# Optimization experiments

Hardware: AMD Instinct MI355X
Metric: run time of the kernel (lower is better)

## Reference

```python
import jax, jax.numpy as jnp
import numpy as np

N_NODES = 50000
N_EDGES = 1_600_000


def add_self_loops(edge_index, n):
    loops = jnp.arange(n, dtype=edge_index.dtype)
    return jnp.concatenate([edge_index, jnp.stack([loops, loops])], axis=1)


def gat_layer(x, edge_index, W, a_src, a_dst, b):
    """PyG GATConv (concat=True, negative_slope=0.2, add_self_loops handled by caller)."""
    src, dst = edge_index[0], edge_index[1]
    n = x.shape[0]
    H, C = a_src.shape
    xp = (x @ W).reshape(n, H, C)                       # [N,H,C] transformed features
    al_src = jnp.einsum('nhc,hc->nh', xp, a_src)        # [N,H]
    al_dst = jnp.einsum('nhc,hc->nh', xp, a_dst)        # [N,H]
    logits = jax.nn.leaky_relu(al_src[src] + al_dst[dst], negative_slope=0.2)  # [E,H]
    m = jax.lax.stop_gradient(jax.ops.segment_max(logits, dst, num_segments=n))
    e = jnp.exp(logits - m[dst])                        # stable segment softmax
    denom = jax.ops.segment_sum(e, dst, num_segments=n)
    alpha = e / denom[dst]                              # [E,H]
    out = jax.ops.segment_sum(xp[src] * alpha[:, :, None], dst, num_segments=n)  # [N,H,C]
    return out.reshape(n, H * C) + b


def setup_inputs() -> dict:
    key = jax.random.key(0)
    ks = jax.random.split(key, 11)
    s = 0.1  # weight scale
    return {
        'x': jax.random.normal(ks[0], (N_NODES, 128), jnp.float32),
        'edge_index': jax.random.randint(ks[1], (2, N_EDGES), 0, N_NODES, jnp.int32),
        'W1': s * jax.random.normal(ks[2], (128, 128), jnp.float32),
        'a_src1': s * jax.random.normal(ks[3], (2, 64), jnp.float32),
        'a_dst1': s * jax.random.normal(ks[4], (2, 64), jnp.float32),
        'b1': s * jax.random.normal(ks[5], (128,), jnp.float32),
        'W2': s * jax.random.normal(ks[6], (128, 64), jnp.float32),
        'a_src2': s * jax.random.normal(ks[7], (2, 32), jnp.float32),
        'a_dst2': s * jax.random.normal(ks[8], (2, 32), jnp.float32),
        'b2': s * jax.random.normal(ks[9], (64,), jnp.float32),
    }


def reference(x, edge_index, W1, a_src1, a_dst1, b1, W2, a_src2, a_dst2, b2):
    ei = add_self_loops(edge_index, x.shape[0])
    encoded = x  # FeatureEncoding with no auxiliary features: identity passthrough
    h = jax.nn.elu(gat_layer(encoded, ei, W1, a_src1, a_dst1, b1))
    out = jax.nn.elu(gat_layer(h, ei, W2, a_src2, a_dst2, b2))
    return (out, encoded)
```

## Files before the change

### kernel.cpp

```cpp
#include <hip/hip_runtime.h>
#include <math.h>

#define N_NODES 50000
#define N_EDGES 1600000
#define EA (N_EDGES + N_NODES)
#define MAXD 128
#define NBUCK 196
#define EPB 4096
#define BCAP 16000

typedef unsigned int uint32;
typedef float f32x4 __attribute__((ext_vector_type(4)));
typedef _Float16 h16x2 __attribute__((ext_vector_type(2)));
typedef _Float16 f16x8 __attribute__((ext_vector_type(8)));

__device__ inline h16x2 u2h(uint32 u) { return __builtin_bit_cast(h16x2, u); }
__device__ inline uint32 h2u(h16x2 h) { return __builtin_bit_cast(uint32, h); }
__device__ inline uint32 pkh(float a, float b) {
  return __builtin_bit_cast(uint32, __builtin_amdgcn_cvt_pkrtz(a, b));
}
__device__ inline ushort f2h(float f) {
  _Float16 h = (_Float16)f;
  return __builtin_bit_cast(ushort, h);
}
__device__ inline int clampi(int v, int lo, int hi) {
  return v < lo ? lo : (v > hi ? hi : v);
}

template<int N, bool AF16, bool COPYX, bool HBLK>
__global__ __launch_bounds__(256) void gemm_mfma_kernel(
    const void* __restrict__ Ap, const float* __restrict__ B,
    const float* __restrict__ asrc, const float* __restrict__ adst,
    ushort* __restrict__ Cb, float* __restrict__ al, float* __restrict__ encout, int M) {
  constexpr int KK = 4;
  constexpr int NC = N / 16;
  constexpr int NH = N / 2;
  __shared__ uint32 Bl[KK * NC * 64 * 4];
  const int t = threadIdx.x;

  for (int id = t; id < KK * NC * 64; id += 256) {
    int lane = id & 63;
    int cf = (id >> 6) % NC;
    int kk = (id >> 6) / NC;
    int col = cf * 16 + (lane & 15);
    int k0 = kk * 32 + (lane >> 4) * 8;
    uint32 w0 = pkh(B[(k0 + 0) * N + col], B[(k0 + 1) * N + col]);
    uint32 w1 = pkh(B[(k0 + 2) * N + col], B[(k0 + 3) * N + col]);
    uint32 w2 = pkh(B[(k0 + 4) * N + col], B[(k0 + 5) * N + col]);
    uint32 w3 = pkh(B[(k0 + 6) * N + col], B[(k0 + 7) * N + col]);
    *reinterpret_cast<uint4*>(&Bl[id * 4]) = make_uint4(w0, w1, w2, w3);
  }
  __syncthreads();

  const int w = t >> 6, lane = t & 63;
  const int l15 = lane & 15, g4 = lane >> 4;
  const int row0 = blockIdx.x * 64 + w * 16;
  int arow = row0 + l15; if (arow > M - 1) arow = M - 1;
  const int k0 = g4 * 8;

  f32x4 acc[NC];
#pragma unroll
  for (int c = 0; c < NC; ++c) acc[c] = f32x4{0.f, 0.f, 0.f, 0.f};

#pragma unroll
  for (int kk = 0; kk < KK; ++kk) {
    f16x8 af;
    if (AF16) {
      int kabs = kk * 32 + k0;
      int kh = kabs >= 64;
      af = *reinterpret_cast<const f16x8*>(
          (const ushort*)Ap + (size_t)kh * N_NODES * 64 + (size_t)arow * 64 + (kabs - kh * 64));
    } else {
      const float* A = (const float*)Ap;
      float4 a0 = *reinterpret_cast<const float4*>(A + (size_t)arow * 128 + kk * 32 + k0);
      float4 a1 = *reinterpret_cast<const float4*>(A + (size_t)arow * 128 + kk * 32 + k0 + 4);
      if (COPYX) {
        *reinterpret_cast<float4*>(encout + (size_t)arow * 128 + kk * 32 + k0)     = a0;
        *reinterpret_cast<float4*>(encout + (size_t)arow * 128 + kk * 32 + k0 + 4) = a1;
      }
      union { uint32 u[4]; f16x8 v; } p;
      p.u[0] = pkh(a0.x, a0.y);
      p.u[1] = pkh(a0.z, a0.w);
      p.u[2] = pkh(a1.x, a1.y);
      p.u[3] = pkh(a1.z, a1.w);
      af = p.v;
    }
#pragma unroll
    for (int c = 0; c < NC; ++c) {
      f16x8 bf = *reinterpret_cast<const f16x8*>(&Bl[((kk * NC + c) * 64 + lane) * 4]);
      acc[c] = __builtin_amdgcn_mfma_f32_16x16x32_f16(af, bf, acc[c], 0, 0, 0);
    }
  }

  float as_c[NC], ad_c[NC];
#pragma unroll
  for (int c = 0; c < NC; ++c) { as_c[c] = asrc[c * 16 + l15]; ad_c[c] = adst[c * 16 + l15]; }
#pragma unroll
  for (int reg = 0; reg < 4; ++reg) {
    int row = row0 + g4 * 4 + reg;
    bool ok = row < M;
    float ps0 = 0.f, ps1 = 0.f, pd0 = 0.f, pd1 = 0.f;
#pragma unroll
    for (int c = 0; c < NC; ++c) {
      float v = acc[c][reg];
      if (ok) {
        int col = c * 16 + l15;
        if (HBLK) {
          int ch = col >= NH;
          Cb[(size_t)ch * N_NODES * NH + (size_t)row * NH + (col - ch * NH)] = f2h(v);
        } else {
          Cb[(size_t)row * N + col] = f2h(v);
        }
      }
      if (c < NC / 2) { ps0 += v * as_c[c]; pd0 += v * ad_c[c]; }
      else            { ps1 += v * as_c[c]; pd1 += v * ad_c[c]; }
    }
#pragma unroll
    for (int off = 8; off >= 1; off >>= 1) {
      ps0 += __shfl_xor(ps0, off); ps1 += __shfl_xor(ps1, off);
      pd0 += __shfl_xor(pd0, off); pd1 += __shfl_xor(pd1, off);
    }
    if (ok && l15 == 0) {
      if (HBLK) {
        ((float2*)al)[row]           = make_float2(ps0, pd0);
        ((float2*)al)[N_NODES + row] = make_float2(ps1, pd1);
      } else {
        *reinterpret_cast<float4*>(&al[row * 4]) = make_float4(ps0, ps1, pd0, pd1);
      }
    }
  }
}

__global__ void partA_kernel(const int* __restrict__ src, const int* __restrict__ dst,
                             int* __restrict__ bcur, uint32* __restrict__ ebuf) {
  __shared__ int h[NBUCK];
  __shared__ int lo[NBUCK];
  __shared__ int rank_[NBUCK];
  __shared__ uint32 staged[EPB];
  const int t = threadIdx.x;
  const int e0 = blockIdx.x * EPB;
  const int ne = min(EPB, N_EDGES - e0);

  for (int i = t; i < NBUCK; i += 256) h[i] = 0;
  __syncthreads();
  for (int i = t; i < ne; i += 256) {
    int d = dst[e0 + i];
    atomicAdd(&h[d >> 8], 1);
  }
  __syncthreads();
  if (t == 0) {
    int a = 0;
    for (int b = 0; b < NBUCK; ++b) { lo[b] = a; a += h[b]; }
  }
  __syncthreads();
  for (int i = t; i < NBUCK; i += 256) rank_[i] = lo[i];
  __syncthreads();
  for (int i = t; i < ne; i += 256) {
    int d = dst[e0 + i];
    int s = src[e0 + i];
    int b = d >> 8;
    int r = atomicAdd(&rank_[b], 1);
    staged[r] = ((uint32)b << 24) | ((uint32)s << 8) | (uint32)(d & 255);
  }
  __syncthreads();
  if (t < NBUCK) {
    int old = atomicAdd(&bcur[t], h[t]);
    rank_[t] = t * BCAP + old - lo[t];
  }
  __syncthreads();
  for (int i = t; i < ne; i += 256) {
    uint32 wd = staged[i];
    ebuf[rank_[wd >> 24] + i] = wd;
  }
}

__global__ __launch_bounds__(256) void partB2_kernel(
    const int* __restrict__ bcur, const uint32* __restrict__ ebuf,
    int* __restrict__ row_start, int* __restrict__ sorted_src) {
  __shared__ uint32 sl[BCAP];
  __shared__ int h[256];
  __shared__ int cur[256];
  __shared__ int wsh[4];
  __shared__ int red[4];
  const int b = blockIdx.x;
  const int t = threadIdx.x, lane = t & 63, wv = t >> 6;
  int myv = 0;
  if (t < b) myv = bcur[t] + min(256, N_NODES - t * 256);
  for (int off = 32; off >= 1; off >>= 1) myv += __shfl_xor(myv, off);
  if (lane == 0) red[wv] = myv;
  h[t] = 0;
  __syncthreads();
  const int bbase = red[0] + red[1] + red[2] + red[3];
  const int base = b * BCAP;
  const int len = min(bcur[b], BCAP);
  for (int i = t; i < len; i += 256) {
    uint32 w = ebuf[base + i];
    sl[i] = w;
    atomicAdd(&h[w & 255], 1);
  }
  __syncthreads();
  const int n = b * 256 + t;
  const bool valid = n < N_NODES;
  int v = valid ? h[t] + 1 : 0;
  int x = v;
  for (int off = 1; off < 64; off <<= 1) {
    int y = __shfl_up(x, off);
    if (lane >= off) x += y;
  }
  if (lane == 63) wsh[wv] = x;
  __syncthreads();
  int wo = 0;
  for (int w = 0; w < wv; ++w) wo += wsh[w];
  int rs = bbase + wo + x - v;
  if (valid) {
    row_start[n] = rs;
    sorted_src[rs] = n;
    cur[t] = rs + 1;
  }
  if (b == 0 && t == 0) row_start[N_NODES] = EA;
  __syncthreads();
  for (int i = t; i < len; i += 256) {
    uint32 w = sl[i];
    int pos = atomicAdd(&cur[w & 255], 1);
    sorted_src[pos] = (int)((w >> 8) & 0xffffu);
  }
}

template<int HCH>
__global__ __launch_bounds__(256) void agg_split_kernel(
    const ushort* __restrict__ xh, const float* __restrict__ al,
    const int* __restrict__ row_start, const int* __restrict__ sorted_src,
    const float* __restrict__ bias, ushort* __restrict__ outp) {
  constexpr int RSH = HCH / 2;
  constexpr int LPR = HCH / 8;
  constexpr int EPI = 64 / LPR;
  constexpr int PF  = 32 / EPI;
  __shared__ uint2 pL[4][MAXD];
  const int gw = (blockIdx.x * blockDim.x + threadIdx.x) >> 6;
  const int lane = threadIdx.x & 63;
  const int wv = (threadIdx.x >> 6) & 3;
  if (gw >= 2 * N_NODES) return;
  const int head = gw >= N_NODES ? 1 : 0;
  const int node = gw - head * N_NODES;
  const float2* alh = (const float2*)al + (size_t)head * N_NODES;
  const uint32* xb32 = (const uint32*)xh + (size_t)head * N_NODES * RSH;
  int start = row_start[node], end = row_start[node + 1];
  start = clampi(start, 0, EA);
  end   = clampi(end, start, EA);
  const int deg = end - start;
  const float adh = alh[node].y;
  const float ESH = 2.7725887f;
  float dsum = 0.f;

  if (deg > MAXD) {
    float m = -1e30f;
    for (int i = start + lane; i < end; i += 64) {
      int s = clampi(sorted_src[i], 0, N_NODES - 1);
      float l = alh[s].x + adh; l = l > 0.f ? l : 0.2f * l;
      m = fmaxf(m, l);
    }
    for (int off = 32; off >= 1; off >>= 1) m = fmaxf(m, __shfl_xor(m, off));
    for (int i = start + lane; i < end; i += 64) {
      int s = clampi(sorted_src[i], 0, N_NODES - 1);
      float l = alh[s].x + adh; l = l > 0.f ? l : 0.2f * l;
      dsum += __expf(l - m);
    }
    for (int off = 32; off >= 1; off >>= 1) dsum += __shfl_xor(dsum, off);
    const float inv = 1.f / dsum;
    if (lane < RSH) {
      float a0 = 0.f, a1 = 0.f;
      for (int i = start; i < end; ++i) {
        int s = clampi(sorted_src[i], 0, N_NODES - 1);
        float l = alh[s].x + adh; l = l > 0.f ? l : 0.2f * l;
        float w = __expf(l - m) * inv;
        h16x2 hx = u2h(xb32[(size_t)s * RSH + lane]);
        a0 = fmaf(w, (float)hx[0], a0);
        a1 = fmaf(w, (float)hx[1], a1);
      }
      int cols0 = head * HCH + lane * 2;
      float o0 = a0 + bias[cols0];
      float o1 = a1 + bias[cols0 + 1];
      o0 = o0 > 0.f ? o0 : __expf(o0) - 1.f;
      o1 = o1 > 0.f ? o1 : __expf(o1) - 1.f;
      ((uint32*)outp)[(size_t)head * N_NODES * RSH + (size_t)node * RSH + lane] = pkh(o0, o1);
    }
    return;
  }

  for (int i = start + lane; i < end; i += 64) {
    int s = clampi(sorted_src[i], 0, N_NODES - 1);
    float l = alh[s].x + adh; l = l > 0.f ? l : 0.2f * l;
    float e = __expf(l - ESH);
    pL[wv][i - start] = make_uint2((uint32)s, pkh(e, e));
    dsum += e;
  }

  const int q  = lane / LPR;
  const int cc = lane % LPR;
  const uint2* myP = &pL[wv][0];
  const uint32* myx = xb32 + cc * 4;

  uint4 pv[PF];
  h16x2 pw[PF];
#pragma unroll
  for (int st = 0; st < PF; ++st) {
    int jj = st * EPI + q;
    int jc = jj < deg ? jj : 0;
    uint2 p = myP[jc];
    pw[st] = u2h(jj < deg ? p.y : 0u);
    pv[st] = *reinterpret_cast<const uint4*>(myx + (size_t)p.x * RSH);
  }

  for (int off = 32; off >= 1; off >>= 1) dsum += __shfl_xor(dsum, off);
  const float inv = 1.f / dsum;

  h16x2 acc2[4];
#pragma unroll
  for (int k = 0; k < 4; ++k) acc2[k] = u2h(0u);

#pragma unroll
  for (int st = 0; st < PF; ++st) {
    acc2[0] += pw[st] * u2h(pv[st].x); acc2[1] += pw[st] * u2h(pv[st].y);
    acc2[2] += pw[st] * u2h(pv[st].z); acc2[3] += pw[st] * u2h(pv[st].w);
  }

  int j = PF * EPI;
  for (; j + 2 * EPI <= deg; j += 2 * EPI) {
    uint2 p0 = myP[j + q];
    uint2 p1 = myP[j + EPI + q];
    const uint4 v0 = *reinterpret_cast<const uint4*>(myx + (size_t)p0.x * RSH);
    const uint4 v1 = *reinterpret_cast<const uint4*>(myx + (size_t)p1.x * RSH);
    h16x2 w0 = u2h(p0.y), w1 = u2h(p1.y);
    acc2[0] += w0 * u2h(v0.x); acc2[1] += w0 * u2h(v0.y);
    acc2[2] += w0 * u2h(v0.z); acc2[3] += w0 * u2h(v0.w);
    acc2[0] += w1 * u2h(v1.x); acc2[1] += w1 * u2h(v1.y);
    acc2[2] += w1 * u2h(v1.z); acc2[3] += w1 * u2h(v1.w);
  }
  for (; j < deg; j += EPI) {
    int jj = j + q;
    int jc = jj < deg ? jj : 0;
    uint2 p = myP[jc];
    h16x2 w2 = u2h(jj < deg ? p.y : 0u);
    const uint4 v = *reinterpret_cast<const uint4*>(myx + (size_t)p.x * RSH);
    acc2[0] += w2 * u2h(v.x); acc2[1] += w2 * u2h(v.y);
    acc2[2] += w2 * u2h(v.z); acc2[3] += w2 * u2h(v.w);
  }

#pragma unroll
  for (int k = 0; k < 4; ++k) {
#pragma unroll
    for (int off = LPR; off < 64; off <<= 1)
      acc2[k] = u2h((uint32)__shfl_xor((int)h2u(acc2[k]), off)) + acc2[k];
  }

  if (q == 0) {
    float o[8];
#pragma unroll
    for (int k = 0; k < 4; ++k) {
      o[2 * k]     = (float)acc2[k][0] * inv + bias[head * HCH + cc * 8 + 2 * k];
      o[2 * k + 1] = (float)acc2[k][1] * inv + bias[head * HCH + cc * 8 + 2 * k + 1];
    }
#pragma unroll
    for (int k = 0; k < 8; ++k) o[k] = o[k] > 0.f ? o[k] : __expf(o[k]) - 1.f;
    uint4 u;
    u.x = pkh(o[0], o[1]); u.y = pkh(o[2], o[3]);
    u.z = pkh(o[4], o[5]); u.w = pkh(o[6], o[7]);
    *reinterpret_cast<uint4*>((uint32*)outp + (size_t)head * N_NODES * RSH +
                              (size_t)node * RSH + cc * 4) = u;
  }
}

__global__ __launch_bounds__(256) void agg_full_kernel(
    const ushort* __restrict__ xh, const float* __restrict__ al,
    const int* __restrict__ row_start, const int* __restrict__ sorted_src,
    const float* __restrict__ bias, float* __restrict__ outp) {
  constexpr int HC = 64;
  constexpr int LPR = HC / 8;
  constexpr int EPI = 64 / LPR;
  constexpr int RS  = HC / 2;
  constexpr int PF  = 4;
  __shared__ uint2 pL[4][2][MAXD];
  const int wid = (blockIdx.x * blockDim.x + threadIdx.x) >> 6;
  const int lane = threadIdx.x & 63;
  const int wv = (threadIdx.x >> 6) & 3;
  if (wid >= N_NODES) return;
  const float4* al4 = (const float4*)al;
  const uint32* xb32 = (const uint32*)xh;
  int start = row_start[wid], end = row_start[wid + 1];
  start = clampi(start, 0, EA);
  end   = clampi(end, start, EA);
  const int deg = end - start;
  float4 mya = al4[wid];
  const float ad0 = mya.z, ad1 = mya.w;
  const float ESH = 2.7725887f;
  float d0 = 0.f, d1 = 0.f;

  if (deg > MAXD) {
    float m0 = -1e30f, m1 = -1e30f;
    for (int i = start + lane; i < end; i += 64) {
      int s = clampi(sorted_src[i], 0, N_NODES - 1);
      float4 a = al4[s];
      float l0 = a.x + ad0; l0 = l0 > 0.f ? l0 : 0.2f * l0;
      float l1 = a.y + ad1; l1 = l1 > 0.f ? l1 : 0.2f * l1;
      m0 = fmaxf(m0, l0); m1 = fmaxf(m1, l1);
    }
    for (int off = 32; off >= 1; off >>= 1) {
      m0 = fmaxf(m0, __shfl_xor(m0, off));
      m1 = fmaxf(m1, __shfl_xor(m1, off));
    }
    for (int i = start + lane; i < end; i += 64) {
      int s = clampi(sorted_src[i], 0, N_NODES - 1);
      float4 a = al4[s];
      float l0 = a.x + ad0; l0 = l0 > 0.f ? l0 : 0.2f * l0;
      float l1 = a.y + ad1; l1 = l1 > 0.f ? l1 : 0.2f * l1;
      d0 += __expf(l0 - m0); d1 += __expf(l1 - m1);
    }
    for (int off = 32; off >= 1; off >>= 1) {
      d0 += __shfl_xor(d0, off);
      d1 += __shfl_xor(d1, off);
    }
    const float inv0 = 1.f / d0, inv1 = 1.f / d1;
    const int cols0 = lane * 2;
    const int head = cols0 >= 32;
    const float invh = head ? inv1 : inv0;
    const float mh = head ? m1 : m0;
    const float adh = head ? ad1 : ad0;
    float a0 = 0.f, a1 = 0.f;
    if (lane < RS) {
      for (int i = start; i < end; ++i) {
        int s = clampi(sorted_src[i], 0, N_NODES - 1);
        float lv = (head ? al4[s].y : al4[s].x) + adh;
        lv = lv > 0.f ? lv : 0.2f * lv;
        float w = __expf(lv - mh) * invh;
        h16x2 hx = u2h(xb32[(size_t)s * RS + lane]);
        a0 = fmaf(w, (float)hx[0], a0);
        a1 = fmaf(w, (float)hx[1], a1);
      }
      float o0 = a0 + bias[cols0];
      float o1 = a1 + bias[cols0 + 1];
      o0 = o0 > 0.f ? o0 : __expf(o0) - 1.f;
      o1 = o1 > 0.f ? o1 : __expf(o1) - 1.f;
      *reinterpret_cast<float2*>(outp + (size_t)wid * HC + cols0) = make_float2(o0, o1);
    }
    return;
  }

  for (int i = start + lane; i < end; i += 64) {
    int s = clampi(sorted_src[i], 0, N_NODES - 1);
    float4 a = al4[s];
    float l0 = a.x + ad0; l0 = l0 > 0.f ? l0 : 0.2f * l0;
    float l1 = a.y + ad1; l1 = l1 > 0.f ? l1 : 0.2f * l1;
    float e0 = __expf(l0 - ESH);
    float e1 = __expf(l1 - ESH);
    int j = i - start;
    pL[wv][0][j] = make_uint2((uint32)s, pkh(e0, e0));
    pL[wv][1][j] = make_uint2((uint32)s, pkh(e1, e1));
    d0 += e0; d1 += e1;
  }

  const int q  = lane / LPR;
  const int cc = lane % LPR;
  const int hd = cc / (LPR / 2);
  const uint2* myP = &pL[wv][hd][0];
  const uint32* myx = xb32 + cc * 4;

  uint4 pv[PF];
  h16x2 pw[PF];
#pragma unroll
  for (int st = 0; st < PF; ++st) {
    int jj = st * EPI + q;
    int jc = jj < deg ? jj : 0;
    uint2 p = myP[jc];
    pw[st] = u2h(jj < deg ? p.y : 0u);
    pv[st] = *reinterpret_cast<const uint4*>(myx + (size_t)p.x * RS);
  }

  for (int off = 32; off >= 1; off >>= 1) {
    d0 += __shfl_xor(d0, off);
    d1 += __shfl_xor(d1, off);
  }
  const float inv0 = 1.f / d0, inv1 = 1.f / d1;

  h16x2 acc2[4];
#pragma unroll
  for (int k = 0; k < 4; ++k) acc2[k] = u2h(0u);

#pragma unroll
  for (int st = 0; st < PF; ++st) {
    acc2[0] += pw[st] * u2h(pv[st].x); acc2[1] += pw[st] * u2h(pv[st].y);
    acc2[2] += pw[st] * u2h(pv[st].z); acc2[3] += pw[st] * u2h(pv[st].w);
  }

  int j = PF * EPI;
  for (; j + 2 * EPI <= deg; j += 2 * EPI) {
    uint2 p0 = myP[j + q];
    uint2 p1 = myP[j + EPI + q];
    const uint4 v0 = *reinterpret_cast<const uint4*>(myx + (size_t)p0.x * RS);
    const uint4 v1 = *reinterpret_cast<const uint4*>(myx + (size_t)p1.x * RS);
    h16x2 w0 = u2h(p0.y), w1 = u2h(p1.y);
    acc2[0] += w0 * u2h(v0.x); acc2[1] += w0 * u2h(v0.y);
    acc2[2] += w0 * u2h(v0.z); acc2[3] += w0 * u2h(v0.w);
    acc2[0] += w1 * u2h(v1.x); acc2[1] += w1 * u2h(v1.y);
    acc2[2] += w1 * u2h(v1.z); acc2[3] += w1 * u2h(v1.w);
  }
  for (; j < deg; j += EPI) {
    int jj = j + q;
    int jc = jj < deg ? jj : 0;
    uint2 p = myP[jc];
    h16x2 w2 = u2h(jj < deg ? p.y : 0u);
    const uint4 v = *reinterpret_cast<const uint4*>(myx + (size_t)p.x * RS);
    acc2[0] += w2 * u2h(v.x); acc2[1] += w2 * u2h(v.y);
    acc2[2] += w2 * u2h(v.z); acc2[3] += w2 * u2h(v.w);
  }

#pragma unroll
  for (int k = 0; k < 4; ++k) {
#pragma unroll
    for (int off = LPR; off < 64; off <<= 1)
      acc2[k] = u2h((uint32)__shfl_xor((int)h2u(acc2[k]), off)) + acc2[k];
  }

  if (q == 0) {
    const float invh = hd ? inv1 : inv0;
    float o[8];
#pragma unroll
    for (int k = 0; k < 4; ++k) {
      o[2 * k]     = (float)acc2[k][0] * invh + bias[cc * 8 + 2 * k];
      o[2 * k + 1] = (float)acc2[k][1] * invh + bias[cc * 8 + 2 * k + 1];
    }
#pragma unroll
    for (int k = 0; k < 8; ++k) o[k] = o[k] > 0.f ? o[k] : __expf(o[k]) - 1.f;
    float* op = outp + (size_t)wid * HC + cc * 8;
    *reinterpret_cast<float4*>(op)     = make_float4(o[0], o[1], o[2], o[3]);
    *reinterpret_cast<float4*>(op + 4) = make_float4(o[4], o[5], o[6], o[7]);
  }
}

extern "C" void kernel_launch(void* const* d_in, const int* in_sizes, int n_in,
                              void* d_out, int out_size, void* d_ws, size_t ws_size,
                              hipStream_t stream) {
  const float* x      = (const float*)d_in[0];
  const int*   ei     = (const int*)d_in[1];
  const float* W1     = (const float*)d_in[2];
  const float* a_src1 = (const float*)d_in[3];
  const float* a_dst1 = (const float*)d_in[4];
  const float* b1     = (const float*)d_in[5];
  const float* W2     = (const float*)d_in[6];
  const float* a_src2 = (const float*)d_in[7];
  const float* a_dst2 = (const float*)d_in[8];
  const float* b2     = (const float*)d_in[9];
  float* out = (float*)d_out;

  char* ws = (char*)d_ws;
  size_t off = 0;
  auto alloc = [&](size_t bytes) {
    void* p = ws + off;
    off = (off + bytes + 255) & ~(size_t)255;
    return p;
  };
  ushort* xh1       = (ushort*)alloc((size_t)N_NODES * 128 * 2);
  ushort* h1h       = (ushort*)alloc((size_t)N_NODES * 128 * 2);
  ushort* xh2       = (ushort*)alloc((size_t)N_NODES * 64 * 2);
  float*  al1       = (float*)alloc((size_t)N_NODES * 4 * 4);
  float*  al2       = (float*)alloc((size_t)N_NODES * 4 * 4);
  int*    row_start = (int*)alloc((size_t)(N_NODES + 1) * 4);
  int*    bcur      = (int*)alloc(NBUCK * 4);
  int*    sorted_src= (int*)alloc((size_t)EA * 4);
  uint32* ebuf      = (uint32*)h1h;

  const int* src = ei;
  const int* dst = ei + N_EDGES;

  const int agg1Blocks = (2 * N_NODES * 64) / 256;
  const int agg2Blocks = (N_NODES * 64) / 256;
  const int partBlocks = (N_EDGES + EPB - 1) / EPB;
  const int gemmBlocks = (N_NODES + 63) / 64;

  hipMemsetAsync(bcur, 0, NBUCK * 4, stream);
  partA_kernel<<<partBlocks, 256, 0, stream>>>(src, dst, bcur, ebuf);
  partB2_kernel<<<NBUCK, 256, 0, stream>>>(bcur, ebuf, row_start, sorted_src);

  gemm_mfma_kernel<128, false, true, true><<<gemmBlocks, 256, 0, stream>>>(
      x, W1, a_src1, a_dst1, xh1, al1, out + (size_t)N_NODES * 64, N_NODES);
  agg_split_kernel<64><<<agg1Blocks, 256, 0, stream>>>(xh1, al1, row_start, sorted_src, b1, h1h);

  gemm_mfma_kernel<64, true, false, false><<<gemmBlocks, 256, 0, stream>>>(
      h1h, W2, a_src2, a_dst2, xh2, al2, nullptr, N_NODES);
  agg_full_kernel<<<agg2Blocks, 256, 0, stream>>>(xh2, al2, row_start, sorted_src, b2, out);
}
```

Measured before the change: 155.2 us.

## Keep per-edge indices and weights in registers via shuffles instead of LDS

For nodes with degree up to 64, each lane now holds one edge's source index and packed softmax weight in registers, and the gather loop broadcasts them with wave shuffles instead of staging them in shared memory. This drops the LDS arrays, cuts LDS traffic and the LDS footprint that limited occupancy, and fully unrolls the gather into at most two batches of four loads per lane. The slow fallback threshold drops from 128 to 64, so nodes with degree between 65 and 128 now take the slower per-lane serial path. Leaky-relu is also rewritten as a single fmaxf.

```diff
diff --git a/kernel.cpp b/kernel.cpp
--- a/kernel.cpp
+++ b/kernel.cpp
@@ -4,7 +4,6 @@
 #define N_NODES 50000
 #define N_EDGES 1600000
 #define EA (N_EDGES + N_NODES)
-#define MAXD 128
 #define NBUCK 196
 #define EPB 4096
 #define BCAP 16000
@@ -234,11 +233,8 @@
   constexpr int RSH = HCH / 2;
   constexpr int LPR = HCH / 8;
   constexpr int EPI = 64 / LPR;
-  constexpr int PF  = 32 / EPI;
-  __shared__ uint2 pL[4][MAXD];
   const int gw = (blockIdx.x * blockDim.x + threadIdx.x) >> 6;
   const int lane = threadIdx.x & 63;
-  const int wv = (threadIdx.x >> 6) & 3;
   if (gw >= 2 * N_NODES) return;
   const int head = gw >= N_NODES ? 1 : 0;
   const int node = gw - head * N_NODES;
@@ -250,19 +246,18 @@
   const int deg = end - start;
   const float adh = alh[node].y;
   const float ESH = 2.7725887f;
-  float dsum = 0.f;
-
-  if (deg > MAXD) {
-    float m = -1e30f;
+
+  if (deg > 64) {
+    float m = -1e30f, dsum = 0.f;
     for (int i = start + lane; i < end; i += 64) {
       int s = clampi(sorted_src[i], 0, N_NODES - 1);
-      float l = alh[s].x + adh; l = l > 0.f ? l : 0.2f * l;
+      float l = alh[s].x + adh; l = fmaxf(l, 0.2f * l);
       m = fmaxf(m, l);
     }
     for (int off = 32; off >= 1; off >>= 1) m = fmaxf(m, __shfl_xor(m, off));
     for (int i = start + lane; i < end; i += 64) {
       int s = clampi(sorted_src[i], 0, N_NODES - 1);
-      float l = alh[s].x + adh; l = l > 0.f ? l : 0.2f * l;
+      float l = alh[s].x + adh; l = fmaxf(l, 0.2f * l);
       dsum += __expf(l - m);
     }
     for (int off = 32; off >= 1; off >>= 1) dsum += __shfl_xor(dsum, off);
@@ -271,7 +266,7 @@
       float a0 = 0.f, a1 = 0.f;
       for (int i = start; i < end; ++i) {
         int s = clampi(sorted_src[i], 0, N_NODES - 1);
-        float l = alh[s].x + adh; l = l > 0.f ? l : 0.2f * l;
+        float l = alh[s].x + adh; l = fmaxf(l, 0.2f * l);
         float w = __expf(l - m) * inv;
         h16x2 hx = u2h(xb32[(size_t)s * RSH + lane]);
         a0 = fmaf(w, (float)hx[0], a0);
@@ -287,70 +282,77 @@
     return;
   }
 
-  for (int i = start + lane; i < end; i += 64) {
-    int s = clampi(sorted_src[i], 0, N_NODES - 1);
-    float l = alh[s].x + adh; l = l > 0.f ? l : 0.2f * l;
-    float e = __expf(l - ESH);
-    pL[wv][i - start] = make_uint2((uint32)s, pkh(e, e));
-    dsum += e;
-  }
+  uint32 s_reg = 0, wpk = 0;
+  float e = 0.f;
+  {
+    int i = start + lane;
+    if (i < end) {
+      int s = clampi(sorted_src[i], 0, N_NODES - 1);
+      s_reg = (uint32)s;
+      float l = alh[s].x + adh;
+      l = fmaxf(l, 0.2f * l);
+      e = __expf(l - ESH);
+      wpk = pkh(e, e);
+    }
+  }
+  float dsum = e;
+  for (int off = 32; off >= 1; off >>= 1) dsum += __shfl_xor(dsum, off);
+  const float inv = 1.f / dsum;
 
   const int q  = lane / LPR;
   const int cc = lane % LPR;
-  const uint2* myP = &pL[wv][0];
   const uint32* myx = xb32 + cc * 4;
 
-  uint4 pv[PF];
-  h16x2 pw[PF];
-#pragma unroll
-  for (int st = 0; st < PF; ++st) {
-    int jj = st * EPI + q;
-    int jc = jj < deg ? jj : 0;
-    uint2 p = myP[jc];
-    pw[st] = u2h(jj < deg ? p.y : 0u);
-    pv[st] = *reinterpret_cast<const uint4*>(myx + (size_t)p.x * RSH);
-  }
-
-  for (int off = 32; off >= 1; off >>= 1) dsum += __shfl_xor(dsum, off);
-  const float inv = 1.f / dsum;
-
   h16x2 acc2[4];
 #pragma unroll
   for (int k = 0; k < 4; ++k) acc2[k] = u2h(0u);
 
-#pragma unroll
-  for (int st = 0; st < PF; ++st) {
-    acc2[0] += pw[st] * u2h(pv[st].x); acc2[1] += pw[st] * u2h(pv[st].y);
-    acc2[2] += pw[st] * u2h(pv[st].z); acc2[3] += pw[st] * u2h(pv[st].w);
-  }
-
-  int j = PF * EPI;
-  for (; j + 2 * EPI <= deg; j += 2 * EPI) {
-    uint2 p0 = myP[j + q];
-    uint2 p1 = myP[j + EPI + q];
-    const uint4 v0 = *reinterpret_cast<const uint4*>(myx + (size_t)p0.x * RSH);
-    const uint4 v1 = *reinterpret_cast<const uint4*>(myx + (size_t)p1.x * RSH);
-    h16x2 w0 = u2h(p0.y), w1 = u2h(p1.y);
-    acc2[0] += w0 * u2h(v0.x); acc2[1] += w0 * u2h(v0.y);
-    acc2[2] += w0 * u2h(v0.z); acc2[3] += w0 * u2h(v0.w);
-    acc2[0] += w1 * u2h(v1.x); acc2[1] += w1 * u2h(v1.y);
-    acc2[2] += w1 * u2h(v1.z); acc2[3] += w1 * u2h(v1.w);
-  }
-  for (; j < deg; j += EPI) {
-    int jj = j + q;
-    int jc = jj < deg ? jj : 0;
-    uint2 p = myP[jc];
-    h16x2 w2 = u2h(jj < deg ? p.y : 0u);
-    const uint4 v = *reinterpret_cast<const uint4*>(myx + (size_t)p.x * RSH);
-    acc2[0] += w2 * u2h(v.x); acc2[1] += w2 * u2h(v.y);
-    acc2[2] += w2 * u2h(v.z); acc2[3] += w2 * u2h(v.w);
+  {
+    int b0 = q, b1 = q + EPI, b2 = q + 2 * EPI, b3 = q + 3 * EPI;
+    uint32 s0 = (uint32)__shfl((int)s_reg, b0), w0 = (uint32)__shfl((int)wpk, b0);
+    uint32 s1 = (uint32)__shfl((int)s_reg, b1), w1 = (uint32)__shfl((int)wpk, b1);
+    uint32 s2 = (uint32)__shfl((int)s_reg, b2), w2 = (uint32)__shfl((int)wpk, b2);
+    uint32 s3 = (uint32)__shfl((int)s_reg, b3), w3 = (uint32)__shfl((int)wpk, b3);
+    const uint4 v0 = *reinterpret_cast<const uint4*>(myx + (size_t)s0 * RSH);
+    const uint4 v1 = *reinterpret_cast<const uint4*>(myx + (size_t)s1 * RSH);
+    const uint4 v2 = *reinterpret_cast<const uint4*>(myx + (size_t)s2 * RSH);
+    const uint4 v3 = *reinterpret_cast<const uint4*>(myx + (size_t)s3 * RSH);
+    h16x2 h0 = u2h(w0), h1 = u2h(w1), h2 = u2h(w2), h3 = u2h(w3);
+    acc2[0] += h0 * u2h(v0.x); acc2[1] += h0 * u2h(v0.y);
+    acc2[2] += h0 * u2h(v0.z); acc2[3] += h0 * u2h(v0.w);
+    acc2[0] += h1 * u2h(v1.x); acc2[1] += h1 * u2h(v1.y);
+    acc2[2] += h1 * u2h(v1.z); acc2[3] += h1 * u2h(v1.w);
+    acc2[0] += h2 * u2h(v2.x); acc2[1] += h2 * u2h(v2.y);
+    acc2[2] += h2 * u2h(v2.z); acc2[3] += h2 * u2h(v2.w);
+    acc2[0] += h3 * u2h(v3.x); acc2[1] += h3 * u2h(v3.y);
+    acc2[2] += h3 * u2h(v3.z); acc2[3] += h3 * u2h(v3.w);
+  }
+  if (deg > 32) {
+    int b0 = 32 + q, b1 = 40 + q, b2 = 48 + q, b3 = 56 + q;
+    uint32 s0 = (uint32)__shfl((int)s_reg, b0), w0 = (uint32)__shfl((int)wpk, b0);
+    uint32 s1 = (uint32)__shfl((int)s_reg, b1), w1 = (uint32)__shfl((int)wpk, b1);
+    uint32 s2 = (uint32)__shfl((int)s_reg, b2), w2 = (uint32)__shfl((int)wpk, b2);
+    uint32 s3 = (uint32)__shfl((int)s_reg, b3), w3 = (uint32)__shfl((int)wpk, b3);
+    const uint4 v0 = *reinterpret_cast<const uint4*>(myx + (size_t)s0 * RSH);
+    const uint4 v1 = *reinterpret_cast<const uint4*>(myx + (size_t)s1 * RSH);
+    const uint4 v2 = *reinterpret_cast<const uint4*>(myx + (size_t)s2 * RSH);
+    const uint4 v3 = *reinterpret_cast<const uint4*>(myx + (size_t)s3 * RSH);
+    h16x2 h0 = u2h(w0), h1 = u2h(w1), h2 = u2h(w2), h3 = u2h(w3);
+    acc2[0] += h0 * u2h(v0.x); acc2[1] += h0 * u2h(v0.y);
+    acc2[2] += h0 * u2h(v0.z); acc2[3] += h0 * u2h(v0.w);
+    acc2[0] += h1 * u2h(v1.x); acc2[1] += h1 * u2h(v1.y);
+    acc2[2] += h1 * u2h(v1.z); acc2[3] += h1 * u2h(v1.w);
+    acc2[0] += h2 * u2h(v2.x); acc2[1] += h2 * u2h(v2.y);
+    acc2[2] += h2 * u2h(v2.z); acc2[3] += h2 * u2h(v2.w);
+    acc2[0] += h3 * u2h(v3.x); acc2[1] += h3 * u2h(v3.y);
+    acc2[2] += h3 * u2h(v3.z); acc2[3] += h3 * u2h(v3.w);
   }
 
 #pragma unroll
   for (int k = 0; k < 4; ++k) {
-#pragma unroll
-    for (int off = LPR; off < 64; off <<= 1)
-      acc2[k] = u2h((uint32)__shfl_xor((int)h2u(acc2[k]), off)) + acc2[k];
+    acc2[k] = u2h((uint32)__shfl_xor((int)h2u(acc2[k]), 8)) + acc2[k];
+    acc2[k] = u2h((uint32)__shfl_xor((int)h2u(acc2[k]), 16)) + acc2[k];
+    acc2[k] = u2h((uint32)__shfl_xor((int)h2u(acc2[k]), 32)) + acc2[k];
   }
 
   if (q == 0) {
@@ -378,11 +380,8 @@
   constexpr int LPR = HC / 8;
   constexpr int EPI = 64 / LPR;
   constexpr int RS  = HC / 2;
-  constexpr int PF  = 4;
-  __shared__ uint2 pL[4][2][MAXD];
   const int wid = (blockIdx.x * blockDim.x + threadIdx.x) >> 6;
   const int lane = threadIdx.x & 63;
-  const int wv = (threadIdx.x >> 6) & 3;
   if (wid >= N_NODES) return;
   const float4* al4 = (const float4*)al;
   const uint32* xb32 = (const uint32*)xh;
@@ -393,15 +392,14 @@
   float4 mya = al4[wid];
   const float ad0 = mya.z, ad1 = mya.w;
   const float ESH = 2.7725887f;
-  float d0 = 0.f, d1 = 0.f;
-
-  if (deg > MAXD) {
-    float m0 = -1e30f, m1 = -1e30f;
+
+  if (deg > 64) {
+    float m0 = -1e30f, m1 = -1e30f, d0 = 0.f, d1 = 0.f;
     for (int i = start + lane; i < end; i += 64) {
       int s = clampi(sorted_src[i], 0, N_NODES - 1);
       float4 a = al4[s];
-      float l0 = a.x + ad0; l0 = l0 > 0.f ? l0 : 0.2f * l0;
-      float l1 = a.y + ad1; l1 = l1 > 0.f ? l1 : 0.2f * l1;
+      float l0 = a.x + ad0; l0 = fmaxf(l0, 0.2f * l0);
+      float l1 = a.y + ad1; l1 = fmaxf(l1, 0.2f * l1);
       m0 = fmaxf(m0, l0); m1 = fmaxf(m1, l1);
     }
     for (int off = 32; off >= 1; off >>= 1) {
@@ -411,8 +409,8 @@
     for (int i = start + lane; i < end; i += 64) {
       int s = clampi(sorted_src[i], 0, N_NODES - 1);
       float4 a = al4[s];
-      float l0 = a.x + ad0; l0 = l0 > 0.f ? l0 : 0.2f * l0;
-      float l1 = a.y + ad1; l1 = l1 > 0.f ? l1 : 0.2f * l1;
+      float l0 = a.x + ad0; l0 = fmaxf(l0, 0.2f * l0);
+      float l1 = a.y + ad1; l1 = fmaxf(l1, 0.2f * l1);
       d0 += __expf(l0 - m0); d1 += __expf(l1 - m1);
     }
     for (int off = 32; off >= 1; off >>= 1) {
@@ -425,12 +423,12 @@
     const float invh = head ? inv1 : inv0;
     const float mh = head ? m1 : m0;
     const float adh = head ? ad1 : ad0;
-    float a0 = 0.f, a1 = 0.f;
     if (lane < RS) {
+      float a0 = 0.f, a1 = 0.f;
       for (int i = start; i < end; ++i) {
         int s = clampi(sorted_src[i], 0, N_NODES - 1);
         float lv = (head ? al4[s].y : al4[s].x) + adh;
-        lv = lv > 0.f ? lv : 0.2f * lv;
+        lv = fmaxf(lv, 0.2f * lv);
         float w = __expf(lv - mh) * invh;
         h16x2 hx = u2h(xb32[(size_t)s * RS + lane]);
         a0 = fmaf(w, (float)hx[0], a0);
@@ -445,79 +443,72 @@
     return;
   }
 
-  for (int i = start + lane; i < end; i += 64) {
-    int s = clampi(sorted_src[i], 0, N_NODES - 1);
-    float4 a = al4[s];
-    float l0 = a.x + ad0; l0 = l0 > 0.f ? l0 : 0.2f * l0;
-    float l1 = a.y + ad1; l1 = l1 > 0.f ? l1 : 0.2f * l1;
-    float e0 = __expf(l0 - ESH);
-    float e1 = __expf(l1 - ESH);
-    int j = i - start;
-    pL[wv][0][j] = make_uint2((uint32)s, pkh(e0, e0));
-    pL[wv][1][j] = make_uint2((uint32)s, pkh(e1, e1));
-    d0 += e0; d1 += e1;
-  }
-
-  const int q  = lane / LPR;
-  const int cc = lane % LPR;
-  const int hd = cc / (LPR / 2);
-  const uint2* myP = &pL[wv][hd][0];
-  const uint32* myx = xb32 + cc * 4;
-
-  uint4 pv[PF];
-  h16x2 pw[PF];
-#pragma unroll
-  for (int st = 0; st < PF; ++st) {
-    int jj = st * EPI + q;
-    int jc = jj < deg ? jj : 0;
-    uint2 p = myP[jc];
-    pw[st] = u2h(jj < deg ? p.y : 0u);
-    pv[st] = *reinterpret_cast<const uint4*>(myx + (size_t)p.x * RS);
-  }
-
+  uint32 s_reg = 0, wpk0 = 0, wpk1 = 0;
+  float e0 = 0.f, e1 = 0.f;
+  {
+    int i = start + lane;
+    if (i < end) {
+      int s = clampi(sorted_src[i], 0, N_NODES - 1);
+      s_reg = (uint32)s;
+      float4 a = al4[s];
+      float l0 = a.x + ad0; l0 = fmaxf(l0, 0.2f * l0);
+      float l1 = a.y + ad1; l1 = fmaxf(l1, 0.2f * l1);
+      e0 = __expf(l0 - ESH);
+      e1 = __expf(l1 - ESH);
+      wpk0 = pkh(e0, e0);
+      wpk1 = pkh(e1, e1);
+    }
+  }
+  float d0 = e0, d1 = e1;
   for (int off = 32; off >= 1; off >>= 1) {
     d0 += __shfl_xor(d0, off);
     d1 += __shfl_xor(d1, off);
   }
   const float inv0 = 1.f / d0, inv1 = 1.f / d1;
 
+  const int q  = lane / LPR;
+  const int cc = lane % LPR;
+  const int hd = cc >> 2;
+  const uint32* myx = xb32 + cc * 4;
+
   h16x2 acc2[4];
 #pragma unroll
   for (int k = 0; k < 4; ++k) acc2[k] = u2h(0u);
 
 #pragma unroll
-  for (int st = 0; st < PF; ++st) {
-    acc2[0] += pw[st] * u2h(pv[st].x); acc2[1] += pw[st] * u2h(pv[st].y);
-    acc2[2] += pw[st] * u2h(pv[st].z); acc2[3] += pw[st] * u2h(pv[st].w);
-  }
-
-  int j = PF * EPI;
-  for (; j + 2 * EPI <= deg; j += 2 * EPI) {
-    uint2 p0 = myP[j + q];
-    uint2 p1 = myP[j + EPI + q];
-    const uint4 v0 = *reinterpret_cast<const uint4*>(myx + (size_t)p0.x * RS);
-    const uint4 v1 = *reinterpret_cast<const uint4*>(myx + (size_t)p1.x * RS);
-    h16x2 w0 = u2h(p0.y), w1 = u2h(p1.y);
-    acc2[0] += w0 * u2h(v0.x); acc2[1] += w0 * u2h(v0.y);
-    acc2[2] += w0 * u2h(v0.z); acc2[3] += w0 * u2h(v0.w);
-    acc2[0] += w1 * u2h(v1.x); acc2[1] += w1 * u2h(v1.y);
-    acc2[2] += w1 * u2h(v1.z); acc2[3] += w1 * u2h(v1.w);
-  }
-  for (; j < deg; j += EPI) {
-    int jj = j + q;
-    int jc = jj < deg ? jj : 0;
-    uint2 p = myP[jc];
-    h16x2 w2 = u2h(jj < deg ? p.y : 0u);
-    const uint4 v = *reinterpret_cast<const uint4*>(myx + (size_t)p.x * RS);
-    acc2[0] += w2 * u2h(v.x); acc2[1] += w2 * u2h(v.y);
-    acc2[2] += w2 * u2h(v.z); acc2[3] += w2 * u2h(v.w);
+  for (int bat = 0; bat < 2; ++bat) {
+    if (bat == 1 && deg <= 32) break;
+    int jb = bat * 32;
+    int b0 = jb + q, b1 = jb + 8 + q, b2 = jb + 16 + q, b3 = jb + 24 + q;
+    uint32 s0 = (uint32)__shfl((int)s_reg, b0);
+    uint32 s1 = (uint32)__shfl((int)s_reg, b1);
+    uint32 s2 = (uint32)__shfl((int)s_reg, b2);
+    uint32 s3 = (uint32)__shfl((int)s_reg, b3);
+    uint32 wa0 = (uint32)__shfl((int)wpk0, b0), wb0 = (uint32)__shfl((int)wpk1, b0);
+    uint32 wa1 = (uint32)__shfl((int)wpk0, b1), wb1 = (uint32)__shfl((int)wpk1, b1);
+    uint32 wa2 = (uint32)__shfl((int)wpk0, b2), wb2 = (uint32)__shfl((int)wpk1, b2);
+    uint32 wa3 = (uint32)__shfl((int)wpk0, b3), wb3 = (uint32)__shfl((int)wpk1, b3);
+    const uint4 v0 = *reinterpret_cast<const uint4*>(myx + (size_t)s0 * RS);
+    const uint4 v1 = *reinterpret_cast<const uint4*>(myx + (size_t)s1 * RS);
+    const uint4 v2 = *reinterpret_cast<const uint4*>(myx + (size_t)s2 * RS);
+    const uint4 v3 = *reinterpret_cast<const uint4*>(myx + (size_t)s3 * RS);
+    h16x2 h0 = u2h(hd ? wb0 : wa0), h1 = u2h(hd ? wb1 : wa1);
+    h16x2 h2 = u2h(hd ? wb2 : wa2), h3 = u2h(hd ? wb3 : wa3);
+    acc2[0] += h0 * u2h(v0.x); acc2[1] += h0 * u2h(v0.y);
+    acc2[2] += h0 * u2h(v0.z); acc2[3] += h0 * u2h(v0.w);
+    acc2[0] += h1 * u2h(v1.x); acc2[1] += h1 * u2h(v1.y);
+    acc2[2] += h1 * u2h(v1.z); acc2[3] += h1 * u2h(v1.w);
+    acc2[0] += h2 * u2h(v2.x); acc2[1] += h2 * u2h(v2.y);
+    acc2[2] += h2 * u2h(v2.z); acc2[3] += h2 * u2h(v2.w);
+    acc2[0] += h3 * u2h(v3.x); acc2[1] += h3 * u2h(v3.y);
+    acc2[2] += h3 * u2h(v3.z); acc2[3] += h3 * u2h(v3.w);
   }
 
 #pragma unroll
   for (int k = 0; k < 4; ++k) {
-#pragma unroll
-    for (int off = LPR; off < 64; off <<= 1)
-      acc2[k] = u2h((uint32)__shfl_xor((int)h2u(acc2[k]), off)) + acc2[k];
+    acc2[k] = u2h((uint32)__shfl_xor((int)h2u(acc2[k]), 8)) + acc2[k];
+    acc2[k] = u2h((uint32)__shfl_xor((int)h2u(acc2[k]), 16)) + acc2[k];
+    acc2[k] = u2h((uint32)__shfl_xor((int)h2u(acc2[k]), 32)) + acc2[k];
   }
 
   if (q == 0) {
```

Result: no change. 153.7 us (-1.0%).
